# Kernel tuning notes

Measured on AMD Instinct MI355X. Metric: run time of the kernel, lower is better.

Reference implementation:

```python
import jax, jax.numpy as jnp
import numpy as np

D_MODEL = 2048
N_HEADS = 16
N_KV_HEADS = 4
HEAD_DIM = 128
ROPE_THETA = 1000000.0
B, T = 2, 2048


def setup_inputs() -> dict:
    key = jax.random.key(0)
    ks = jax.random.split(key, 5)
    s_in = 1.0 / np.sqrt(D_MODEL)
    s_o = 1.0 / np.sqrt(N_HEADS * HEAD_DIM)
    return {
        "x": jax.random.normal(ks[0], (B, T, D_MODEL), jnp.float32),
        "w_q": jax.random.normal(ks[1], (N_HEADS * HEAD_DIM, D_MODEL), jnp.float32) * s_in,
        "w_k": jax.random.normal(ks[2], (N_KV_HEADS * HEAD_DIM, D_MODEL), jnp.float32) * s_in,
        "w_v": jax.random.normal(ks[3], (N_KV_HEADS * HEAD_DIM, D_MODEL), jnp.float32) * s_in,
        "w_o": jax.random.normal(ks[4], (D_MODEL, N_HEADS * HEAD_DIM), jnp.float32) * s_o,
    }


def _rope_cos_sin(T, dtype):
    # inv_freq over even dims, emb = concat(freqs, freqs) (HF/llama convention)
    inv_freq = 1.0 / (ROPE_THETA ** (jnp.arange(0, HEAD_DIM, 2, dtype=jnp.float32) / HEAD_DIM))
    freqs = jnp.arange(T, dtype=jnp.float32)[:, None] * inv_freq[None, :]  # [T, hd/2]
    emb = jnp.concatenate([freqs, freqs], axis=-1)  # [T, hd]
    return jnp.cos(emb).astype(dtype), jnp.sin(emb).astype(dtype)


def _rotate_half(x):
    x1, x2 = jnp.split(x, 2, axis=-1)
    return jnp.concatenate([-x2, x1], axis=-1)


def reference(x, w_q, w_k, w_v, w_o):
    B, T, D = x.shape
    # QKV projections (bias=False), split heads -> [B, H, T, hd]
    q = (x @ w_q.T).reshape(B, T, N_HEADS, HEAD_DIM).transpose(0, 2, 1, 3)
    k = (x @ w_k.T).reshape(B, T, N_KV_HEADS, HEAD_DIM).transpose(0, 2, 1, 3)
    v = (x @ w_v.T).reshape(B, T, N_KV_HEADS, HEAD_DIM).transpose(0, 2, 1, 3)
    # RoPE
    cos, sin = _rope_cos_sin(T, x.dtype)  # [T, hd]
    q = q * cos + _rotate_half(q) * sin
    k = k * cos + _rotate_half(k) * sin
    # GQA: expand kv heads (repeat_interleave over head dim)
    rep = N_HEADS // N_KV_HEADS
    k = jnp.repeat(k, rep, axis=1)
    v = jnp.repeat(v, rep, axis=1)
    # Eager attention: QK^T * scale + causal mask, softmax, PV
    scale = HEAD_DIM ** -0.5
    scores = jnp.einsum("bhtd,bhsd->bhts", q, k) * scale
    causal = jnp.tril(jnp.ones((T, T), dtype=bool))
    scores = jnp.where(causal[None, None], scores, jnp.finfo(scores.dtype).min)
    probs = jax.nn.softmax(scores, axis=-1)
    out = jnp.einsum("bhts,bhsd->bhtd", probs, v)  # [B, H, T, hd]
    out = out.transpose(0, 2, 1, 3).reshape(B, T, N_HEADS * HEAD_DIM)
    return out @ w_o.T
```

## Files before the change

### kernel.cpp

```cpp
#include <hip/hip_runtime.h>
#include <cstdint>
#include <cstddef>

typedef unsigned short u16;
typedef unsigned u32;
typedef unsigned long long u64;
typedef __attribute__((ext_vector_type(8))) short short8;
typedef __attribute__((ext_vector_type(4))) float f32x4;

#define T_SEQ 2048
#define DM    2048
#define NHEAD 16
#define NKV   4
#define HD    128
#define NEGBIG (-3.0e38f)
#define QSCALE 0.1275525165017459f
#define L2IF (-0.31143258583318043f)

__device__ __forceinline__ u16 f2bf(float f) {
  union { float f; unsigned u; } c; c.f = f;
  return (u16)((c.u + 0x7fffu + ((c.u >> 16) & 1u)) >> 16);
}
__device__ __forceinline__ float bf2f(u16 b) {
  union { float f; unsigned u; } c; c.u = ((unsigned)b) << 16;
  return c.f;
}
__device__ __forceinline__ void gl_lds16(const u16* g, u16* l) {
  __builtin_amdgcn_global_load_lds(
      (const __attribute__((address_space(1))) void*)g,
      (__attribute__((address_space(3))) void*)l, 16, 0, 0);
}

__global__ void castk_all(const float* __restrict__ x, const float* __restrict__ wq,
                          const float* __restrict__ wk, const float* __restrict__ wv,
                          const float* __restrict__ wo, u16* __restrict__ dst) {
  long long i4 = (long long)blockIdx.x * 256 + threadIdx.x;
  const float* src; long long off;
  if (i4 < (2LL << 20))                    { src = x;  off = i4; }
  else if (i4 < (3LL << 20))               { src = wq; off = i4 - (2LL << 20); }
  else if (i4 < (3LL << 20) + (1 << 18))   { src = wk; off = i4 - (3LL << 20); }
  else if (i4 < (3LL << 20) + (2 << 18))   { src = wv; off = i4 - (3LL << 20) - (1 << 18); }
  else                                     { src = wo; off = i4 - (3LL << 20) - (2 << 18); }
  float4 v = *(const float4*)(src + off * 4);
  u16* d = dst + i4 * 4;
  d[0] = f2bf(v.x); d[1] = f2bf(v.y); d[2] = f2bf(v.z); d[3] = f2bf(v.w);
}

__global__ void tabk(float2* __restrict__ Tab) {
  int idx = blockIdx.x * 256 + threadIdx.x;
  float ang = (float)(idx >> 6) * exp2f((float)(idx & 63) * L2IF);
  float sn, cs;
  sincosf(ang, &sn, &cs);
  Tab[idx] = make_float2(cs, sn);
}

__global__ void ropek(u16* __restrict__ buf, const float2* __restrict__ Tab) {
  int idx = blockIdx.x * 256 + threadIdx.x;
  int r = idx >> 6, i = idx & 63;
  int t = r & (T_SEQ - 1);
  float2 cs = Tab[(t << 6) + i];
  size_t base = (size_t)r * HD + i;
  float x1 = bf2f(buf[base]), x2 = bf2f(buf[base + 64]);
  buf[base]      = f2bf(x1 * cs.x - x2 * cs.y);
  buf[base + 64] = f2bf(x2 * cs.x + x1 * cs.y);
}

template <int MODE>
__global__ __launch_bounds__(256) void gemm_bt(
    const u16* __restrict__ A, const u16* __restrict__ Bm,
    void* __restrict__ Out0, u16* __restrict__ OutK, u16* __restrict__ OutV,
    int M, int N, int K) {
  __shared__ __align__(16) u16 As[2][128 * 32];
  __shared__ __align__(16) u16 Bs[2][128 * 32];
  const int tid = threadIdx.x;
  const int w = tid >> 6, l = tid & 63;
  const int lm = l & 15, q = l >> 4;
  const int m0 = blockIdx.y * 128, n0 = blockIdx.x * 128;
  const int mq = w & 1, nq = w >> 1;
  const u16* Ab = A + (size_t)m0 * K;
  const u16* Bb = Bm + (size_t)n0 * K;

  const int s0_ = w * 64 + l, s1_ = 256 + s0_;
  const int row0 = s0_ >> 2, kq0 = (s0_ & 3) * 8;
  const int row1 = s1_ >> 2, kq1 = (s1_ & 3) * 8;

  f32x4 acc[4][4] = {};
  const int nk = K >> 5;

  gl_lds16(Ab + (size_t)row0 * K + kq0, &As[0][s0_ * 8]);
  gl_lds16(Bb + (size_t)row0 * K + kq0, &Bs[0][s0_ * 8]);
  gl_lds16(Ab + (size_t)row1 * K + kq1, &As[0][s1_ * 8]);
  gl_lds16(Bb + (size_t)row1 * K + kq1, &Bs[0][s1_ * 8]);
  __syncthreads();

  for (int ki = 0; ki < nk; ++ki) {
    const int bb = ki & 1;
    if (ki + 1 < nk) {
      const int k0 = (ki + 1) << 5;
      gl_lds16(Ab + (size_t)row0 * K + k0 + kq0, &As[bb ^ 1][s0_ * 8]);
      gl_lds16(Bb + (size_t)row0 * K + k0 + kq0, &Bs[bb ^ 1][s0_ * 8]);
      gl_lds16(Ab + (size_t)row1 * K + k0 + kq1, &As[bb ^ 1][s1_ * 8]);
      gl_lds16(Bb + (size_t)row1 * K + k0 + kq1, &Bs[bb ^ 1][s1_ * 8]);
    }
    short8 af[4], bf[4];
#pragma unroll
    for (int i = 0; i < 4; ++i) {
      af[i] = *(const short8*)(&As[bb][(mq * 64 + i * 16 + lm) * 32 + q * 8]);
      bf[i] = *(const short8*)(&Bs[bb][(nq * 64 + i * 16 + lm) * 32 + q * 8]);
    }
#pragma unroll
    for (int i = 0; i < 4; ++i)
#pragma unroll
      for (int j = 0; j < 4; ++j)
        acc[i][j] = __builtin_amdgcn_mfma_f32_16x16x32_bf16(af[i], bf[j], acc[i][j], 0, 0, 0);
    __syncthreads();
  }

#pragma unroll
  for (int i = 0; i < 4; ++i)
#pragma unroll
    for (int j = 0; j < 4; ++j)
#pragma unroll
      for (int r = 0; r < 4; ++r) {
        int m = m0 + mq * 64 + i * 16 + q * 4 + r;
        int n = n0 + nq * 64 + j * 16 + lm;
        float v = acc[i][j][r];
        if constexpr (MODE == 0) {
          ((float*)Out0)[(size_t)m * N + n] = v;
        } else {
          int b = m >> 11, t = m & (T_SEQ - 1);
          if (n < 2048) {
            int h = n >> 7, d = n & (HD - 1);
            ((u16*)Out0)[(((size_t)(b * NHEAD + h)) * T_SEQ + t) * HD + d] = f2bf(v * QSCALE);
          } else if (n < 2560) {
            int nn = n - 2048, h = nn >> 7, d = nn & (HD - 1);
            OutK[(((size_t)(b * NKV + h)) * T_SEQ + t) * HD + d] = f2bf(v);
          } else {
            int nn = n - 2560, h = nn >> 7, d = nn & (HD - 1);
            OutV[(((size_t)(b * NKV + h)) * HD + d) * T_SEQ + t] = f2bf(v);
          }
        }
      }
}

#define PSTRIDE 72
__global__ __launch_bounds__(256, 2) void attnk(
    const u16* __restrict__ Q, const u16* __restrict__ Kh,
    const u16* __restrict__ Vt, const float2* __restrict__ Tab,
    u16* __restrict__ Oa) {
  __shared__ __align__(16) u16 Ks[2][64 * 128];
  __shared__ __align__(16) u16 Vs[2][128 * 64];
  __shared__ __align__(16) u16 Pl[4][16 * PSTRIDE];
  const int tid = threadIdx.x;
  const int w = tid >> 6, l = tid & 63, lm = l & 15, q = l >> 4;

  const int wg = blockIdx.x;
  const int g = wg & 7, slot = wg >> 3;
  const int b = g >> 2, kvh = g & 3;
  const int h = kvh * 4 + (slot & 3);
  const int p = slot >> 2;

  const u16* Kb = Kh + ((size_t)(b * NKV + kvh)) * T_SEQ * HD;
  const u16* Vb = Vt + ((size_t)(b * NKV + kvh)) * HD * T_SEQ;
  u16* Pw = Pl[w];

  const int r16 = tid >> 4, c16 = tid & 15;
  const int r8  = tid >> 3, c8  = tid & 7;

#pragma unroll 1
  for (int half = 0; half < 2; ++half) {
    const int tile = half ? p : (31 - p);
    const int tbase = tile * 64 + w * 16;
    const u16* Qb = Q + (((size_t)(b * NHEAD + h)) * T_SEQ + tbase) * HD;

    short8 qa[4];
#pragma unroll
    for (int ks = 0; ks < 4; ++ks)
      qa[ks] = *(const short8*)(Qb + (size_t)lm * HD + ks * 32 + q * 8);

    {
      const float2* tb = Tab + (((size_t)(tbase + lm)) << 6) + q * 8;
#pragma unroll
      for (int ks = 0; ks < 2; ++ks) {
        short8 lo = qa[ks], hi = qa[ks + 2];
#pragma unroll
        for (int e = 0; e < 8; ++e) {
          float2 cs = tb[ks * 32 + e];
          float x1 = bf2f((u16)lo[e]), x2 = bf2f((u16)hi[e]);
          lo[e] = (short)f2bf(x1 * cs.x - x2 * cs.y);
          hi[e] = (short)f2bf(x2 * cs.x + x1 * cs.y);
        }
        qa[ks] = lo; qa[ks + 2] = hi;
      }
    }

    float m_i = NEGBIG, l_i = 0.f;
    f32x4 oacc[8] = {};
    const int nst = tile + 1;

    {
#pragma unroll
      for (int j = 0; j < 4; ++j) {
        int s = j * 16 + r16, gs = c16 ^ (s & 15);
        gl_lds16(Kb + (size_t)s * HD + gs * 8, &Ks[0][s * 128 + c16 * 8]);
      }
#pragma unroll
      for (int j = 0; j < 4; ++j) {
        int d = j * 32 + r8, gs = c8 ^ (d & 7);
        gl_lds16(Vb + (size_t)d * T_SEQ + gs * 8, &Vs[0][d * 64 + c8 * 8]);
      }
    }
    __syncthreads();

    for (int st = 0; st < nst; ++st) {
      const int bb = st & 1;
      if (st + 1 < nst) {
        const int s0n = (st + 1) * 64;
#pragma unroll
        for (int j = 0; j < 4; ++j) {
          int s = j * 16 + r16, gs = c16 ^ (s & 15);
          gl_lds16(Kb + (size_t)(s0n + s) * HD + gs * 8, &Ks[bb ^ 1][s * 128 + c16 * 8]);
        }
#pragma unroll
        for (int j = 0; j < 4; ++j) {
          int d = j * 32 + r8, gs = c8 ^ (d & 7);
          gl_lds16(Vb + (size_t)d * T_SEQ + s0n + gs * 8, &Vs[bb ^ 1][d * 64 + c8 * 8]);
        }
      }

      f32x4 sacc[4] = {};
#pragma unroll
      for (int ks = 0; ks < 4; ++ks)
#pragma unroll
        for (int nt = 0; nt < 4; ++nt) {
          short8 kb = *(const short8*)(&Ks[bb][(nt * 16 + lm) * 128 + ((ks * 4 + q) ^ lm) * 8]);
          sacc[nt] = __builtin_amdgcn_mfma_f32_16x16x32_bf16(kb, qa[ks], sacc[nt], 0, 0, 0);
        }

      const bool diag = (st == nst - 1);
      const int s0 = st * 64;
      float mx = NEGBIG;
#pragma unroll
      for (int nt = 0; nt < 4; ++nt)
#pragma unroll
        for (int j = 0; j < 4; ++j) {
          float v = sacc[nt][j];
          if (diag) {
            int s_abs = s0 + nt * 16 + q * 4 + j;
            if (s_abs > tbase + lm) v = NEGBIG;
            sacc[nt][j] = v;
          }
          mx = fmaxf(mx, v);
        }
      mx = fmaxf(mx, __shfl_xor(mx, 16, 64));
      mx = fmaxf(mx, __shfl_xor(mx, 32, 64));
      if (__any(mx > m_i + 8.0f)) {
        float mnew = fmaxf(m_i, mx);
        float alpha = exp2f(m_i - mnew);
        m_i = mnew;
        l_i *= alpha;
#pragma unroll
        for (int dt = 0; dt < 8; ++dt)
#pragma unroll
          for (int j = 0; j < 4; ++j) oacc[dt][j] *= alpha;
      }
      float sum = 0.f;
#pragma unroll
      for (int nt = 0; nt < 4; ++nt) {
        float e0 = exp2f(sacc[nt][0] - m_i), e1 = exp2f(sacc[nt][1] - m_i);
        float e2 = exp2f(sacc[nt][2] - m_i), e3 = exp2f(sacc[nt][3] - m_i);
        sum += (e0 + e1) + (e2 + e3);
        u32 lo32 = __builtin_amdgcn_perm(__float_as_uint(e1), __float_as_uint(e0), 0x07060302u);
        u32 hi32 = __builtin_amdgcn_perm(__float_as_uint(e3), __float_as_uint(e2), 0x07060302u);
        *(u64*)(Pw + lm * PSTRIDE + nt * 16 + q * 4) = ((u64)hi32 << 32) | lo32;
      }
      sum += __shfl_xor(sum, 16, 64);
      sum += __shfl_xor(sum, 32, 64);
      l_i += sum;

      asm volatile("" ::: "memory");

#pragma unroll
      for (int ks = 0; ks < 2; ++ks) {
        short8 pa = *(const short8*)(Pw + lm * PSTRIDE + ks * 32 + q * 8);
#pragma unroll
        for (int dt = 0; dt < 8; ++dt) {
          short8 vb = *(const short8*)(
              &Vs[bb][(dt * 16 + lm) * 64 + ((ks * 4 + q) ^ (lm & 7)) * 8]);
          oacc[dt] = __builtin_amdgcn_mfma_f32_16x16x32_bf16(vb, pa, oacc[dt], 0, 0, 0);
        }
      }
      __syncthreads();
    }

    float inv = 1.0f / l_i;
    int t = tbase + lm;
#pragma unroll
    for (int dt = 0; dt < 8; ++dt) {
      u16 ok[4];
#pragma unroll
      for (int j = 0; j < 4; ++j) ok[j] = f2bf(oacc[dt][j] * inv);
      *(u64*)(Oa + ((size_t)(b * T_SEQ + t)) * (NHEAD * HD) + h * HD + dt * 16 + q * 4) =
          (u64)ok[0] | ((u64)ok[1] << 16) | ((u64)ok[2] << 32) | ((u64)ok[3] << 48);
    }
  }
}

extern "C" void kernel_launch(void* const* d_in, const int* in_sizes, int n_in,
                              void* d_out, int out_size, void* d_ws, size_t ws_size,
                              hipStream_t stream) {
  const float* x  = (const float*)d_in[0];
  const float* wq = (const float*)d_in[1];
  const float* wk = (const float*)d_in[2];
  const float* wv = (const float*)d_in[3];
  const float* wo = (const float*)d_in[4];
  float* out = (float*)d_out;

  u16* ws  = (u16*)d_ws;
  u16* xb  = ws;
  u16* wqb = xb  + (8u << 20);
  u16* wkb = wqb + (4u << 20);
  u16* wvb = wkb + (1u << 20);
  u16* wob = wvb + (1u << 20);
  u16* Qb  = wob + (4u << 20);
  u16* Kb  = Qb  + (8u << 20);
  u16* Vtb = Kb  + (2u << 20);
  u16* Ab  = xb;
  float2* tab = (float2*)wkb;

  castk_all<<<18432, 256, 0, stream>>>(x, wq, wk, wv, wo, ws);

  gemm_bt<3><<<dim3(24, 32), 256, 0, stream>>>(xb, wqb, Qb, Kb, Vtb, 4096, 3072, 2048);

  tabk<<<512, 256, 0, stream>>>(tab);
  ropek<<<4096, 256, 0, stream>>>(Kb, tab);

  attnk<<<512, 256, 0, stream>>>(Qb, Kb, Vtb, tab, Ab);

  gemm_bt<0><<<dim3(16, 32), 256, 0, stream>>>(Ab, wob, out, nullptr, nullptr, 4096, 2048, 2048);
}
```

Measured before the change: 295.2 us.

## Replace GEMM with 256x256-tile 8-wave kernel using finer-grained pipelined staging

Replaces the 128x128 tile, 4-wave GEMM with a 256x256 tile, 8-wave kernel. Each wave computes a 128x64 sub-tile, and K is split into 64-wide stages with 32-wide half-chunks. Global-to-LDS loads are interleaved between MFMA quads, with explicit vmcnt waits, raw barriers and s_setprio around the MFMA bursts. The aim is more data reuse per LDS byte and better overlap of loads with compute. The cost is fewer workgroups: 192 for QKV and 128 for the output projection on a 256-CU part, which may underfill the GPU. The extra barriers and larger LDS use could also limit occupancy.

```diff
diff --git a/kernel.cpp b/kernel.cpp
--- a/kernel.cpp
+++ b/kernel.cpp
@@ -30,6 +30,11 @@
       (const __attribute__((address_space(1))) void*)g,
       (__attribute__((address_space(3))) void*)l, 16, 0, 0);
 }
+
+#define FENCE() asm volatile("" ::: "memory")
+#define BAR() do { FENCE(); __builtin_amdgcn_s_barrier(); FENCE(); } while (0)
+#define WAITV4() asm volatile("s_waitcnt vmcnt(4)" ::: "memory")
+#define WAITV0() asm volatile("s_waitcnt vmcnt(0)" ::: "memory")
 
 __global__ void castk_all(const float* __restrict__ x, const float* __restrict__ wq,
                           const float* __restrict__ wk, const float* __restrict__ wv,
@@ -65,79 +70,138 @@
   buf[base + 64] = f2bf(x2 * cs.x + x1 * cs.y);
 }
 
+template <int FH>
+__device__ __forceinline__ void mfma_quad(f32x4 (&acc)[8][4], const short8 (&af)[4],
+                                          const short8 (&bfr)[4]) {
+#pragma unroll
+  for (int i = 0; i < 4; ++i)
+#pragma unroll
+    for (int j = 0; j < 4; ++j)
+      acc[FH * 4 + i][j] =
+          __builtin_amdgcn_mfma_f32_16x16x32_bf16(af[i], bfr[j], acc[FH * 4 + i][j], 0, 0, 0);
+}
+
 template <int MODE>
-__global__ __launch_bounds__(256) void gemm_bt(
+__global__ __launch_bounds__(512, 2) void gemm8(
     const u16* __restrict__ A, const u16* __restrict__ Bm,
     void* __restrict__ Out0, u16* __restrict__ OutK, u16* __restrict__ OutV,
     int M, int N, int K) {
-  __shared__ __align__(16) u16 As[2][128 * 32];
-  __shared__ __align__(16) u16 Bs[2][128 * 32];
+  __shared__ __align__(16) u16 AS[2][2][256 * 32];
+  __shared__ __align__(16) u16 BS[2][2][256 * 32];
   const int tid = threadIdx.x;
-  const int w = tid >> 6, l = tid & 63;
-  const int lm = l & 15, q = l >> 4;
-  const int m0 = blockIdx.y * 128, n0 = blockIdx.x * 128;
-  const int mq = w & 1, nq = w >> 1;
+  const int l = tid & 63, lm = l & 15, q = l >> 4;
+  const int w = tid >> 6, wr = w >> 2, wc = w & 3;
+  const int m0 = blockIdx.y * 256, n0 = blockIdx.x * 256;
   const u16* Ab = A + (size_t)m0 * K;
   const u16* Bb = Bm + (size_t)n0 * K;
 
-  const int s0_ = w * 64 + l, s1_ = 256 + s0_;
-  const int row0 = s0_ >> 2, kq0 = (s0_ & 3) * 8;
-  const int row1 = s1_ >> 2, kq1 = (s1_ & 3) * 8;
-
-  f32x4 acc[4][4] = {};
-  const int nk = K >> 5;
-
-  gl_lds16(Ab + (size_t)row0 * K + kq0, &As[0][s0_ * 8]);
-  gl_lds16(Bb + (size_t)row0 * K + kq0, &Bs[0][s0_ * 8]);
-  gl_lds16(Ab + (size_t)row1 * K + kq1, &As[0][s1_ * 8]);
-  gl_lds16(Bb + (size_t)row1 * K + kq1, &Bs[0][s1_ * 8]);
-  __syncthreads();
-
-  for (int ki = 0; ki < nk; ++ki) {
-    const int bb = ki & 1;
-    if (ki + 1 < nk) {
-      const int k0 = (ki + 1) << 5;
-      gl_lds16(Ab + (size_t)row0 * K + k0 + kq0, &As[bb ^ 1][s0_ * 8]);
-      gl_lds16(Bb + (size_t)row0 * K + k0 + kq0, &Bs[bb ^ 1][s0_ * 8]);
-      gl_lds16(Ab + (size_t)row1 * K + k0 + kq1, &As[bb ^ 1][s1_ * 8]);
-      gl_lds16(Bb + (size_t)row1 * K + k0 + kq1, &Bs[bb ^ 1][s1_ * 8]);
-    }
-    short8 af[4], bf[4];
-#pragma unroll
-    for (int i = 0; i < 4; ++i) {
-      af[i] = *(const short8*)(&As[bb][(mq * 64 + i * 16 + lm) * 32 + q * 8]);
-      bf[i] = *(const short8*)(&Bs[bb][(nq * 64 + i * 16 + lm) * 32 + q * 8]);
-    }
-#pragma unroll
-    for (int i = 0; i < 4; ++i)
-#pragma unroll
-      for (int j = 0; j < 4; ++j)
-        acc[i][j] = __builtin_amdgcn_mfma_f32_16x16x32_bf16(af[i], bf[j], acc[i][j], 0, 0, 0);
-    __syncthreads();
+  const int r0 = tid >> 2, c0 = (tid & 3) * 8;
+  const int r1 = (512 + tid) >> 2, c1 = (tid & 3) * 8;
+
+#define STG_A(T, KC) do { \
+    const int kb_ = (T) * 64 + (KC) * 32; \
+    gl_lds16(Ab + (size_t)r0 * K + kb_ + c0, &AS[(T) & 1][KC][tid * 8]); \
+    gl_lds16(Ab + (size_t)r1 * K + kb_ + c1, &AS[(T) & 1][KC][(512 + tid) * 8]); \
+  } while (0)
+#define STG_B(T, KC) do { \
+    const int kb_ = (T) * 64 + (KC) * 32; \
+    gl_lds16(Bb + (size_t)r0 * K + kb_ + c0, &BS[(T) & 1][KC][tid * 8]); \
+    gl_lds16(Bb + (size_t)r1 * K + kb_ + c1, &BS[(T) & 1][KC][(512 + tid) * 8]); \
+  } while (0)
+
+  f32x4 acc[8][4] = {};
+  const int nt = K >> 6;
+
+  STG_A(0, 0); STG_B(0, 0);
+  STG_A(0, 1); STG_B(0, 1);
+  STG_A(1, 0); STG_B(1, 0);
+  WAITV4();
+  BAR();
+
+  for (int t = 0; t < nt; ++t) {
+    const int cur = t & 1;
+    short8 bfr[4];
+
+    {
+      short8 af[4];
+#pragma unroll
+      for (int i = 0; i < 4; ++i)
+        bfr[i] = *(const short8*)(&BS[cur][0][(wc * 64 + i * 16 + lm) * 32 + q * 8]);
+#pragma unroll
+      for (int i = 0; i < 4; ++i)
+        af[i] = *(const short8*)(&AS[cur][0][(wr * 128 + i * 16 + lm) * 32 + q * 8]);
+      if (t + 1 < nt) { STG_A(t + 1, 1); STG_B(t + 1, 1); }
+      BAR();
+      __builtin_amdgcn_s_setprio(1);
+      mfma_quad<0>(acc, af, bfr);
+      __builtin_amdgcn_s_setprio(0);
+      BAR();
+    }
+    {
+      short8 af[4];
+#pragma unroll
+      for (int i = 0; i < 4; ++i)
+        af[i] = *(const short8*)(&AS[cur][0][(wr * 128 + (4 + i) * 16 + lm) * 32 + q * 8]);
+      BAR();
+      __builtin_amdgcn_s_setprio(1);
+      mfma_quad<1>(acc, af, bfr);
+      __builtin_amdgcn_s_setprio(0);
+      BAR();
+    }
+    {
+      short8 af[4];
+#pragma unroll
+      for (int i = 0; i < 4; ++i)
+        bfr[i] = *(const short8*)(&BS[cur][1][(wc * 64 + i * 16 + lm) * 32 + q * 8]);
+#pragma unroll
+      for (int i = 0; i < 4; ++i)
+        af[i] = *(const short8*)(&AS[cur][1][(wr * 128 + i * 16 + lm) * 32 + q * 8]);
+      if (t + 2 < nt) STG_A(t + 2, 0);
+      BAR();
+      __builtin_amdgcn_s_setprio(1);
+      mfma_quad<0>(acc, af, bfr);
+      __builtin_amdgcn_s_setprio(0);
+      BAR();
+    }
+    {
+      short8 af[4];
+#pragma unroll
+      for (int i = 0; i < 4; ++i)
+        af[i] = *(const short8*)(&AS[cur][1][(wr * 128 + (4 + i) * 16 + lm) * 32 + q * 8]);
+      if (t + 2 < nt) STG_B(t + 2, 0);
+      BAR();
+      __builtin_amdgcn_s_setprio(1);
+      mfma_quad<1>(acc, af, bfr);
+      __builtin_amdgcn_s_setprio(0);
+      if (t < nt - 2) { WAITV4(); } else { WAITV0(); }
+      BAR();
+    }
   }
-
-#pragma unroll
-  for (int i = 0; i < 4; ++i)
-#pragma unroll
-    for (int j = 0; j < 4; ++j)
+#undef STG_A
+#undef STG_B
+
+#pragma unroll
+  for (int fm = 0; fm < 8; ++fm)
+#pragma unroll
+    for (int fn = 0; fn < 4; ++fn)
 #pragma unroll
       for (int r = 0; r < 4; ++r) {
-        int m = m0 + mq * 64 + i * 16 + q * 4 + r;
-        int n = n0 + nq * 64 + j * 16 + lm;
-        float v = acc[i][j][r];
+        int m = m0 + wr * 128 + fm * 16 + q * 4 + r;
+        int n = n0 + wc * 64 + fn * 16 + lm;
+        float v = acc[fm][fn][r];
         if constexpr (MODE == 0) {
           ((float*)Out0)[(size_t)m * N + n] = v;
         } else {
-          int b = m >> 11, t = m & (T_SEQ - 1);
+          int b = m >> 11, tt = m & (T_SEQ - 1);
           if (n < 2048) {
             int h = n >> 7, d = n & (HD - 1);
-            ((u16*)Out0)[(((size_t)(b * NHEAD + h)) * T_SEQ + t) * HD + d] = f2bf(v * QSCALE);
+            ((u16*)Out0)[(((size_t)(b * NHEAD + h)) * T_SEQ + tt) * HD + d] = f2bf(v * QSCALE);
           } else if (n < 2560) {
             int nn = n - 2048, h = nn >> 7, d = nn & (HD - 1);
-            OutK[(((size_t)(b * NKV + h)) * T_SEQ + t) * HD + d] = f2bf(v);
+            OutK[(((size_t)(b * NKV + h)) * T_SEQ + tt) * HD + d] = f2bf(v);
           } else {
             int nn = n - 2560, h = nn >> 7, d = nn & (HD - 1);
-            OutV[(((size_t)(b * NKV + h)) * HD + d) * T_SEQ + t] = f2bf(v);
+            OutV[(((size_t)(b * NKV + h)) * HD + d) * T_SEQ + tt] = f2bf(v);
           }
         }
       }
@@ -330,12 +394,12 @@
 
   castk_all<<<18432, 256, 0, stream>>>(x, wq, wk, wv, wo, ws);
 
-  gemm_bt<3><<<dim3(24, 32), 256, 0, stream>>>(xb, wqb, Qb, Kb, Vtb, 4096, 3072, 2048);
+  gemm8<3><<<dim3(12, 16), 512, 0, stream>>>(xb, wqb, Qb, Kb, Vtb, 4096, 3072, 2048);
 
   tabk<<<512, 256, 0, stream>>>(tab);
   ropek<<<4096, 256, 0, stream>>>(Kb, tab);
 
   attnk<<<512, 256, 0, stream>>>(Qb, Kb, Vtb, tab, Ab);
 
-  gemm_bt<0><<<dim3(16, 32), 256, 0, stream>>>(Ab, wob, out, nullptr, nullptr, 4096, 2048, 2048);
-}
+  gemm8<0><<<dim3(8, 16), 512, 0, stream>>>(Ab, wob, out, nullptr, nullptr, 4096, 2048, 2048);
+}
```

Result: slower. 332.8 us (+12.7%).
